# Optimization experiments

Measured on AMD Instinct MI355X. Metric: run time of the kernel, lower is better.

The kernel has to match this reference:

```python
import jax, jax.numpy as jnp
import numpy as np

B = 2_000_000
ND = 3

def _skew(v):
    # v: [B,3] -> [B,3,3] skew-symmetric matrix
    z = jnp.zeros_like(v[..., 0])
    r0 = jnp.stack([z, -v[..., 2], v[..., 1]], axis=-1)
    r1 = jnp.stack([v[..., 2], z, -v[..., 0]], axis=-1)
    r2 = jnp.stack([-v[..., 1], v[..., 0], z], axis=-1)
    return jnp.stack([r0, r1, r2], axis=-2)

def _rotmat(v):
    # Closed-form expm of skew(v) (Rodrigues). Mathematically identical to tf.linalg.expm.
    th2 = jnp.sum(v * v, axis=-1)                      # [B]
    th = jnp.sqrt(th2)
    small = th < 1e-6
    th_s = jnp.where(small, 1.0, th)
    th2_s = jnp.where(small, 1.0, th2)
    a = jnp.where(small, 1.0, jnp.sin(th) / th_s)      # sin(t)/t
    b = jnp.where(small, 0.5, (1.0 - jnp.cos(th)) / th2_s)  # (1-cos t)/t^2
    K = _skew(v)                                       # [B,3,3]
    I = jnp.eye(ND, dtype=v.dtype)
    return I + a[:, None, None] * K + b[:, None, None] * jnp.matmul(K, K)

def setup_inputs() -> dict:
    key = jax.random.key(0)
    k1, k2, k3, k4 = jax.random.split(key, 4)
    trans = jax.random.normal(k1, (B, ND), dtype=jnp.float32)
    rotat = jax.random.normal(k2, (B, ND), dtype=jnp.float32)
    scal_dir = jax.random.normal(k3, (B, ND), dtype=jnp.float32)
    scal = jax.random.normal(k4, (B, ND), dtype=jnp.float32)
    return {"trans": trans, "rotat": rotat, "scal_dir": scal_dir, "scal": scal}

def reference(trans, rotat, scal_dir, scal):
    R = _rotmat(rotat)          # [B,3,3] rotation
    U = _rotmat(scal_dir)       # [B,3,3] scaling direction
    D = jnp.exp(scal)           # expm(diag(s)) == diag(exp(s)), [B,3]
    # U @ diag(D) @ U^T, then R @ (.)
    Ut = jnp.swapaxes(U, -1, -2)
    M = jnp.matmul(U, D[:, :, None] * Ut)   # diag(D) @ U^T broadcast as row-scaling
    M = jnp.matmul(R, M)
    return jnp.concatenate([M, trans[:, :, None]], axis=2)  # [B,3,4]
```

## Files before the change

### kernel.cpp

```cpp
#include <hip/hip_runtime.h>
#include <math.h>

#define TPB 256

struct __align__(4) f3 { float x, y, z; };

__device__ __forceinline__ void rodrigues(float v0, float v1, float v2, float R[9]) {
    float th2 = v0 * v0 + v1 * v1 + v2 * v2;
    float th  = sqrtf(th2);
    float s, c;
    sincosf(th, &s, &c);
    bool  sm = th < 1e-6f;
    float a  = sm ? 1.0f : s / th;
    float b  = sm ? 0.5f : (1.0f - c) / th2;
    float cc = 1.0f - b * th2;
    R[0] = cc + b * v0 * v0;      R[1] = b * v0 * v1 - a * v2;  R[2] = b * v0 * v2 + a * v1;
    R[3] = b * v0 * v1 + a * v2;  R[4] = cc + b * v1 * v1;      R[5] = b * v1 * v2 - a * v0;
    R[6] = b * v0 * v2 - a * v1;  R[7] = b * v1 * v2 + a * v0;  R[8] = cc + b * v2 * v2;
}

__device__ __forceinline__ void compute_store(
    const f3 t, const f3 r, const f3 u, const f3 s, float4* __restrict__ o)
{
    float R[9], U[9];
    rodrigues(r.x, r.y, r.z, R);
    rodrigues(u.x, u.y, u.z, U);
    const float d0 = expf(s.x), d1 = expf(s.y), d2 = expf(s.z);

    const float W0 = U[0]*d0, W1 = U[1]*d1, W2 = U[2]*d2;
    const float W3 = U[3]*d0, W4 = U[4]*d1, W5 = U[5]*d2;
    const float W6 = U[6]*d0, W7 = U[7]*d1, W8 = U[8]*d2;

    const float S00 = W0*U[0] + W1*U[1] + W2*U[2];
    const float S01 = W0*U[3] + W1*U[4] + W2*U[5];
    const float S02 = W0*U[6] + W1*U[7] + W2*U[8];
    const float S11 = W3*U[3] + W4*U[4] + W5*U[5];
    const float S12 = W3*U[6] + W4*U[7] + W5*U[8];
    const float S22 = W6*U[6] + W7*U[7] + W8*U[8];

    const float M00 = R[0]*S00 + R[1]*S01 + R[2]*S02;
    const float M01 = R[0]*S01 + R[1]*S11 + R[2]*S12;
    const float M02 = R[0]*S02 + R[1]*S12 + R[2]*S22;
    const float M10 = R[3]*S00 + R[4]*S01 + R[5]*S02;
    const float M11 = R[3]*S01 + R[4]*S11 + R[5]*S12;
    const float M12 = R[3]*S02 + R[4]*S12 + R[5]*S22;
    const float M20 = R[6]*S00 + R[7]*S01 + R[8]*S02;
    const float M21 = R[6]*S01 + R[7]*S11 + R[8]*S12;
    const float M22 = R[6]*S02 + R[7]*S12 + R[8]*S22;

    o[0] = make_float4(M00, M01, M02, t.x);
    o[1] = make_float4(M10, M11, M12, t.y);
    o[2] = make_float4(M20, M21, M22, t.z);
}

__global__ __launch_bounds__(TPB) void aff_kernel(
    const f3* __restrict__ trans,
    const f3* __restrict__ rotat,
    const f3* __restrict__ sdir,
    const f3* __restrict__ scal,
    float4* __restrict__ out,
    int B)
{
    const int lane  = threadIdx.x & 63;
    const int wid   = (blockIdx.x * TPB + threadIdx.x) >> 6;
    const int ebase = wid << 8;
    if (ebase >= B) return;

    const int e0 = ebase + lane;
    const bool g1 = (ebase +  64) < B;
    const bool g2 = (ebase + 128) < B;
    const bool g3 = (ebase + 192) < B;

    f3 tA, rA, uA, sA;
    f3 tB, rB, uB, sB;

    { const int e = e0;      tA = trans[e]; rA = rotat[e]; uA = sdir[e]; sA = scal[e]; }
    if (g1) { const int e = e0 + 64;  tB = trans[e]; rB = rotat[e]; uB = sdir[e]; sB = scal[e]; }

    compute_store(tA, rA, uA, sA, out + 3 * e0);
    if (g2) { const int e = e0 + 128; tA = trans[e]; rA = rotat[e]; uA = sdir[e]; sA = scal[e]; }

    if (g1) compute_store(tB, rB, uB, sB, out + 3 * (e0 + 64));
    if (g3) { const int e = e0 + 192; tB = trans[e]; rB = rotat[e]; uB = sdir[e]; sB = scal[e]; }

    if (g2) compute_store(tA, rA, uA, sA, out + 3 * (e0 + 128));
    if (g3) compute_store(tB, rB, uB, sB, out + 3 * (e0 + 192));
}

extern "C" void kernel_launch(void* const* d_in, const int* in_sizes, int n_in,
                              void* d_out, int out_size, void* d_ws, size_t ws_size,
                              hipStream_t stream) {
    int B = in_sizes[0] / 3;
    int waves  = (B + 255) / 256;
    int blocks = (waves * 64 + TPB - 1) / TPB;
    aff_kernel<<<blocks, TPB, 0, stream>>>((const f3*)d_in[0], (const f3*)d_in[1],
                                           (const f3*)d_in[2], (const f3*)d_in[3],
                                           (float4*)d_out, B);
}
```

Baseline: 184.3 us.

## Batch eight elements per thread and issue all loads before compute

Replaces the two-slot software pipeline (four elements per wave-lane) with a block-strided scheme where each thread loads eight elements' inputs up front, then computes and stores them. This aims to expose more outstanding memory requests per thread to hide load latency. It increases register pressure, which may reduce occupancy, and reduces the number of blocks launched.

```diff
diff --git a/kernel.cpp b/kernel.cpp
--- a/kernel.cpp
+++ b/kernel.cpp
@@ -2,6 +2,7 @@
 #include <math.h>
 
 #define TPB 256
+#define NB  8
 
 struct __align__(4) f3 { float x, y, z; };
 
@@ -61,38 +62,40 @@
     float4* __restrict__ out,
     int B)
 {
-    const int lane  = threadIdx.x & 63;
-    const int wid   = (blockIdx.x * TPB + threadIdx.x) >> 6;
-    const int ebase = wid << 8;
-    if (ebase >= B) return;
+    const int tid = threadIdx.x;
+    const int E   = blockIdx.x * (TPB * NB);
 
-    const int e0 = ebase + lane;
-    const bool g1 = (ebase +  64) < B;
-    const bool g2 = (ebase + 128) < B;
-    const bool g3 = (ebase + 192) < B;
+    f3 t[NB], r[NB], u[NB], s[NB];
+    bool g[NB];
 
-    f3 tA, rA, uA, sA;
-    f3 tB, rB, uB, sB;
+#pragma unroll
+    for (int b = 0; b < NB; ++b) {
+        const int e = E + b * TPB + tid;
+        g[b] = (e < B);
+        if (g[b]) {
+            t[b] = trans[e];
+            r[b] = rotat[e];
+            u[b] = sdir [e];
+            s[b] = scal [e];
+        } else {
+            t[b] = f3{0.f,0.f,0.f}; r[b] = t[b]; u[b] = t[b]; s[b] = t[b];
+        }
+    }
 
-    { const int e = e0;      tA = trans[e]; rA = rotat[e]; uA = sdir[e]; sA = scal[e]; }
-    if (g1) { const int e = e0 + 64;  tB = trans[e]; rB = rotat[e]; uB = sdir[e]; sB = scal[e]; }
-
-    compute_store(tA, rA, uA, sA, out + 3 * e0);
-    if (g2) { const int e = e0 + 128; tA = trans[e]; rA = rotat[e]; uA = sdir[e]; sA = scal[e]; }
-
-    if (g1) compute_store(tB, rB, uB, sB, out + 3 * (e0 + 64));
-    if (g3) { const int e = e0 + 192; tB = trans[e]; rB = rotat[e]; uB = sdir[e]; sB = scal[e]; }
-
-    if (g2) compute_store(tA, rA, uA, sA, out + 3 * (e0 + 128));
-    if (g3) compute_store(tB, rB, uB, sB, out + 3 * (e0 + 192));
+#pragma unroll
+    for (int b = 0; b < NB; ++b) {
+        if (g[b]) {
+            const int e = E + b * TPB + tid;
+            compute_store(t[b], r[b], u[b], s[b], out + 3 * e);
+        }
+    }
 }
 
 extern "C" void kernel_launch(void* const* d_in, const int* in_sizes, int n_in,
                               void* d_out, int out_size, void* d_ws, size_t ws_size,
                               hipStream_t stream) {
     int B = in_sizes[0] / 3;
-    int waves  = (B + 255) / 256;
-    int blocks = (waves * 64 + TPB - 1) / TPB;
+    int blocks = (B + TPB * NB - 1) / (TPB * NB);
     aff_kernel<<<blocks, TPB, 0, stream>>>((const f3*)d_in[0], (const f3*)d_in[1],
                                            (const f3*)d_in[2], (const f3*)d_in[3],
                                            (float4*)d_out, B);
```

Result: slower. 190.6 us (+3.5%).
